# Performance work log

Hardware: AMD Instinct MI355X
Metric: run time of the kernel (lower is better)

Reference implementation:

```python
import jax, jax.numpy as jnp
import numpy as np


def setup_inputs() -> dict:
    key = jax.random.key(0)
    kq, kk, kv, kl = jax.random.split(key, 4)
    B, H, S, D = 2, 8, 1024, 64
    Q = jax.random.normal(kq, (B, H, S, D), dtype=jnp.float32)
    K = jax.random.normal(kk, (B, H, S, D), dtype=jnp.float32)
    V = jax.random.normal(kv, (B, H, S, D), dtype=jnp.float32)
    valid_lens = jax.random.randint(kl, (B, S), 0, S, dtype=jnp.int64)
    return {"Q": Q, "K": K, "V": V, "valid_lens": valid_lens}


def reference(Q, K, V, valid_lens):
    # Q,K,V: [B,H,S,D]. The torch repeat/reshape makes K[b,i,j]=K[b,j],
    # i.e. every query head i attends to every key/value head j.
    B, H, S, D = Q.shape
    inv_sqrt = 1.0 / jnp.sqrt(jnp.asarray(D, dtype=Q.dtype))
    # score[b,i,j,s,t] = Q[b,i,s,:] . K[b,j,t,:] / sqrt(D)
    score = jnp.einsum('bisd,bjtd->bijst', Q, K) * inv_sqrt
    attention_weights = jax.nn.softmax(score, axis=-1)  # [B,H,H,S,S]
    # ctx[b,i,s,d] = sum_j sum_t w[b,i,j,s,t] * V[b,j,t,d]  (matmul then sum over j)
    ctx = jnp.einsum('bijst,bjtd->bisd', attention_weights, V)  # [B,H,S,D]
    context = jnp.transpose(ctx, (0, 2, 1, 3)).reshape(B, S, H * D)  # [B,S,H*D]
    return context, attention_weights
```

## Files before the change

### kernel.cpp

```cpp
#include <hip/hip_runtime.h>
#include <hip/hip_bf16.h>

#define B_ 2
#define H_ 8
#define S_ 1024
#define D_ 64
#define PLP 136
#define STRIPH (16 * PLP)

typedef short short8 __attribute__((ext_vector_type(8)));
typedef float f32x4 __attribute__((ext_vector_type(4)));
typedef float f32x2 __attribute__((ext_vector_type(2)));

__device__ __forceinline__ unsigned int f2bf(float f) {
  union { float f; unsigned int u; } v; v.f = f;
  return (v.u + 0x7fffu + ((v.u >> 16) & 1u)) >> 16;
}
__device__ __forceinline__ float bf2f(unsigned int bits) {
  union { unsigned int u; float f; } v; v.u = bits << 16;
  return v.f;
}
__device__ __forceinline__ unsigned int cvt_pk_bf16(float lo, float hi) {
  unsigned int r;
  asm("v_cvt_pk_bf16_f32 %0, %1, %2" : "=v"(r) : "v"(lo), "v"(hi));
  return r;
}

__global__ void conv_bf16_kernel(const float* __restrict__ src,
                                 unsigned short* __restrict__ dst, int n4) {
  int idx = blockIdx.x * blockDim.x + threadIdx.x;
  if (idx >= n4) return;
  const float4 v = ((const float4*)src)[idx];
  unsigned int lo = f2bf(v.x) | (f2bf(v.y) << 16);
  unsigned int hi = f2bf(v.z) | (f2bf(v.w) << 16);
  ((uint2*)dst)[idx] = make_uint2(lo, hi);
}

__global__ void transpose_v_kernel(const float* __restrict__ V,
                                   unsigned short* __restrict__ Vt) {
  __shared__ float tile[64][65];
  int bh = blockIdx.x >> 4;
  int t0 = (blockIdx.x & 15) * 64;
  int tid = threadIdx.x;
  int cx = tid & 63, ry = tid >> 6;
  const float* src = V + ((size_t)bh * S_ + t0) * D_;
#pragma unroll
  for (int r = 0; r < 16; ++r) {
    int row = r * 4 + ry;
    tile[row][cx] = src[(size_t)row * D_ + cx];
  }
  __syncthreads();
  unsigned short* dst = Vt + (size_t)bh * D_ * S_ + t0;
#pragma unroll
  for (int r = 0; r < 16; ++r) {
    int d = r * 4 + ry;
    dst[(size_t)d * S_ + cx] = (unsigned short)f2bf(tile[cx][d]);
  }
}

__global__ __launch_bounds__(512, 2) void attn_kernel(
    const unsigned short* __restrict__ Qb,
    const unsigned short* __restrict__ Kb,
    const unsigned short* __restrict__ Vt,
    float* __restrict__ w_out,
    float* __restrict__ ctx_out)
{
  const int tid  = threadIdx.x;
  const int w    = tid >> 6;
  const int lane = tid & 63;
  const int g = lane >> 4;
  const int c = lane & 15;
  const int raw = blockIdx.x;
  const int bid = (raw & 7) * 32 + (raw >> 3);
  const int sb = bid & 15;
  const int i  = (bid >> 4) & 7;
  const int b  = bid >> 7;
  const int s0 = sb * 64;
  const int t0 = w * 128;

  __shared__ __align__(16) unsigned short pstrips[32 * STRIPH];
  __shared__ float ssum[2][8][64];
  unsigned short* stripA = pstrips + (4 * w) * STRIPH;
  unsigned short* stripB = stripA + STRIPH;
  unsigned short* stripC = stripB + STRIPH;
  unsigned short* stripD = stripC + STRIPH;

  const unsigned short* qrow =
      Qb + ((size_t)((b * H_ + i) * S_) + s0 + c) * D_ + g * 8;
  short8 qa0 = *(const short8*)(qrow);
  short8 qa1 = *(const short8*)(qrow + 32);
  short8 qb0 = *(const short8*)(qrow + 16 * D_);
  short8 qb1 = *(const short8*)(qrow + 16 * D_ + 32);
  short8 qc0 = *(const short8*)(qrow + 32 * D_);
  short8 qc1 = *(const short8*)(qrow + 32 * D_ + 32);
  short8 qd0 = *(const short8*)(qrow + 48 * D_);
  short8 qd1 = *(const short8*)(qrow + 48 * D_ + 32);

  f32x4 ctxA[4], ctxB[4], ctxC[4], ctxD[4];
#pragma unroll
  for (int nt = 0; nt < 4; ++nt) {
    ctxA[nt] = (f32x4){0.f, 0.f, 0.f, 0.f};
    ctxB[nt] = (f32x4){0.f, 0.f, 0.f, 0.f};
    ctxC[nt] = (f32x4){0.f, 0.f, 0.f, 0.f};
    ctxD[nt] = (f32x4){0.f, 0.f, 0.f, 0.f};
  }

  const float SC = 0.18033688011112042f;

  for (int j = 0; j < H_; ++j) {
    const int par = j & 1;
    const unsigned short* kbase = Kb + (size_t)((b * H_ + j) * S_) * D_;

    float rsA = 0.f, rsB = 0.f, rsC = 0.f, rsD = 0.f;
#pragma unroll
    for (int tt = 0; tt < 8; ++tt) {
      const unsigned short* kr = kbase + (size_t)(t0 + tt * 16 + c) * D_ + g * 8;
      short8 kf0 = *(const short8*)(kr);
      short8 kf1 = *(const short8*)(kr + 32);
#define PASS1_HALF(QF0, QF1, RS, STRIPP)                                      \
      {                                                                       \
        f32x4 acc = (f32x4){0.f, 0.f, 0.f, 0.f};                              \
        acc = __builtin_amdgcn_mfma_f32_16x16x32_bf16(kf0, QF0, acc, 0, 0, 0);\
        acc = __builtin_amdgcn_mfma_f32_16x16x32_bf16(kf1, QF1, acc, 0, 0, 0);\
        float e0 = exp2f(acc[0] * SC);                                        \
        float e1 = exp2f(acc[1] * SC);                                        \
        float e2 = exp2f(acc[2] * SC);                                        \
        float e3 = exp2f(acc[3] * SC);                                        \
        RS += (e0 + e1) + (e2 + e3);                                          \
        uint2 pk = make_uint2(cvt_pk_bf16(e0, e1), cvt_pk_bf16(e2, e3));      \
        *(uint2*)&STRIPP[c * PLP + tt * 16 + 4 * g] = pk;                     \
      }
      PASS1_HALF(qa0, qa1, rsA, stripA)
      PASS1_HALF(qb0, qb1, rsB, stripB)
      PASS1_HALF(qc0, qc1, rsC, stripC)
      PASS1_HALF(qd0, qd1, rsD, stripD)
#undef PASS1_HALF
    }
    rsA += __shfl_xor(rsA, 16, 64);
    rsA += __shfl_xor(rsA, 32, 64);
    rsB += __shfl_xor(rsB, 16, 64);
    rsB += __shfl_xor(rsB, 32, 64);
    rsC += __shfl_xor(rsC, 16, 64);
    rsC += __shfl_xor(rsC, 32, 64);
    rsD += __shfl_xor(rsD, 16, 64);
    rsD += __shfl_xor(rsD, 32, 64);
    if (lane < 16) {
      ssum[par][w][lane]      = rsA;
      ssum[par][w][16 + lane] = rsB;
      ssum[par][w][32 + lane] = rsC;
      ssum[par][w][48 + lane] = rsD;
    }

    f32x4 pvA[4], pvB[4], pvC[4], pvD[4];
#pragma unroll
    for (int nt = 0; nt < 4; ++nt) {
      pvA[nt] = (f32x4){0.f, 0.f, 0.f, 0.f};
      pvB[nt] = (f32x4){0.f, 0.f, 0.f, 0.f};
      pvC[nt] = (f32x4){0.f, 0.f, 0.f, 0.f};
      pvD[nt] = (f32x4){0.f, 0.f, 0.f, 0.f};
    }
    const unsigned short* vbase =
        Vt + ((size_t)((b * H_ + j) * D_) + c) * S_ + t0 + g * 8;
#pragma unroll
    for (int ch = 0; ch < 4; ++ch) {
      short8 paA = *(const short8*)&stripA[c * PLP + ch * 32 + g * 8];
      short8 paB = *(const short8*)&stripB[c * PLP + ch * 32 + g * 8];
      short8 paC = *(const short8*)&stripC[c * PLP + ch * 32 + g * 8];
      short8 paD = *(const short8*)&stripD[c * PLP + ch * 32 + g * 8];
#pragma unroll
      for (int nt = 0; nt < 4; ++nt) {
        short8 vf = *(const short8*)(vbase + (size_t)nt * 16 * S_ + ch * 32);
        pvA[nt] = __builtin_amdgcn_mfma_f32_16x16x32_bf16(paA, vf, pvA[nt], 0, 0, 0);
        pvB[nt] = __builtin_amdgcn_mfma_f32_16x16x32_bf16(paB, vf, pvB[nt], 0, 0, 0);
        pvC[nt] = __builtin_amdgcn_mfma_f32_16x16x32_bf16(paC, vf, pvC[nt], 0, 0, 0);
        pvD[nt] = __builtin_amdgcn_mfma_f32_16x16x32_bf16(paD, vf, pvD[nt], 0, 0, 0);
      }
    }

    asm volatile("s_waitcnt lgkmcnt(0)\n\ts_barrier" ::: "memory");

#define ROWSUM(OFS)                                                           \
    (ssum[par][0][(OFS) + c] + ssum[par][1][(OFS) + c] +                      \
     ssum[par][2][(OFS) + c] + ssum[par][3][(OFS) + c] +                      \
     ssum[par][4][(OFS) + c] + ssum[par][5][(OFS) + c] +                      \
     ssum[par][6][(OFS) + c] + ssum[par][7][(OFS) + c])
    float iqA = 1.f / ROWSUM(0);
    float iqB = 1.f / ROWSUM(16);
    float iqC = 1.f / ROWSUM(32);
    float iqD = 1.f / ROWSUM(48);
#undef ROWSUM

#define CTX_SCALE(IQ, PV, CTX)                                                \
    {                                                                         \
      float r0 = __shfl(IQ, 4 * g + 0, 64);                                   \
      float r1 = __shfl(IQ, 4 * g + 1, 64);                                   \
      float r2 = __shfl(IQ, 4 * g + 2, 64);                                   \
      float r3 = __shfl(IQ, 4 * g + 3, 64);                                   \
      _Pragma("unroll")                                                       \
      for (int nt = 0; nt < 4; ++nt) {                                        \
        CTX[nt][0] += PV[nt][0] * r0;                                         \
        CTX[nt][1] += PV[nt][1] * r1;                                         \
        CTX[nt][2] += PV[nt][2] * r2;                                         \
        CTX[nt][3] += PV[nt][3] * r3;                                         \
      }                                                                       \
    }
    CTX_SCALE(iqA, pvA, ctxA)
    CTX_SCALE(iqB, pvB, ctxB)
    CTX_SCALE(iqC, pvC, ctxC)
    CTX_SCALE(iqD, pvD, ctxD)
#undef CTX_SCALE

    float* wbase = w_out +
        ((size_t)((b * H_ + i) * H_ + j) * S_ + s0) * S_ + t0 + lane * 2;
#define WSTORE_HALF(IQ, STRIPP, ROWOFS)                                       \
    _Pragma("unroll")                                                         \
    for (int rr = 0; rr < 16; ++rr) {                                         \
      const float iq =                                                        \
          __uint_as_float(__builtin_amdgcn_readlane(__float_as_uint(IQ), rr));\
      unsigned int pk = *(const unsigned int*)&STRIPP[rr * PLP + lane * 2];   \
      f32x2 ww;                                                               \
      ww[0] = bf2f(pk & 0xffffu) * iq;                                        \
      ww[1] = bf2f(pk >> 16)     * iq;                                        \
      __builtin_nontemporal_store(                                            \
          ww, (f32x2*)(wbase + (size_t)((ROWOFS) + rr) * S_));                \
    }
    WSTORE_HALF(iqA, stripA, 0)
    WSTORE_HALF(iqB, stripB, 16)
    WSTORE_HALF(iqC, stripC, 32)
    WSTORE_HALF(iqD, stripD, 48)
#undef WSTORE_HALF
  }

  __syncthreads();
  float (*ctile)[64][68] = (float(*)[64][68])pstrips;
#pragma unroll
  for (int nt = 0; nt < 4; ++nt)
#pragma unroll
    for (int r = 0; r < 4; ++r) {
      ctile[w][4 * g + r][nt * 16 + c]      = ctxA[nt][r];
      ctile[w][16 + 4 * g + r][nt * 16 + c] = ctxB[nt][r];
      ctile[w][32 + 4 * g + r][nt * 16 + c] = ctxC[nt][r];
      ctile[w][48 + 4 * g + r][nt * 16 + c] = ctxD[nt][r];
    }
  __syncthreads();
#pragma unroll
  for (int it = 0; it < 2; ++it) {
    const int slot = it * 512 + tid;
    const int r  = slot >> 4;
    const int d0 = (slot & 15) * 4;
    f32x4 s = *(const f32x4*)&ctile[0][r][d0];
#pragma unroll
    for (int e = 1; e < 8; ++e) s += *(const f32x4*)&ctile[e][r][d0];
    *(f32x4*)(ctx_out + ((size_t)(b * S_ + s0 + r) * (H_ * D_) + i * D_ + d0)) = s;
  }
}

extern "C" void kernel_launch(void* const* d_in, const int* in_sizes, int n_in,
                              void* d_out, int out_size, void* d_ws, size_t ws_size,
                              hipStream_t stream) {
  const float* Q = (const float*)d_in[0];
  const float* K = (const float*)d_in[1];
  const float* V = (const float*)d_in[2];

  const size_t nelem = (size_t)B_ * H_ * S_ * D_;
  float* outc = (float*)d_out;
  float* outw = outc + (size_t)B_ * S_ * H_ * D_;

  unsigned short* Qb = (unsigned short*)d_ws;
  unsigned short* Kb = Qb + nelem;
  unsigned short* Vt = Kb + nelem;

  conv_bf16_kernel<<<1024, 256, 0, stream>>>(Q, Qb, (int)(nelem / 4));
  conv_bf16_kernel<<<1024, 256, 0, stream>>>(K, Kb, (int)(nelem / 4));
  transpose_v_kernel<<<256, 256, 0, stream>>>(V, Vt);

  attn_kernel<<<B_ * H_ * (S_ / 64), 512, 0, stream>>>(Qb, Kb, Vt, outw, outc);
}
```

Baseline: 157.6 us.

## Fuse prologue kernels and interleave weight stores with PV MFMAs

Merges the two bf16 conversion kernels and the V transpose into a single prologue launch, removing two kernel launches. In the attention kernel, the row-sum barrier and reciprocal now come before the PV matmul, and the normalized attention-weight stores are issued per chunk between the MFMA groups. The aim is to overlap the large global write stream with tensor-core work. Stores also widen from 2-float to 4-float nontemporal writes covering two rows per wave. The price is a longer barrier wait before the PV work and extra readlane/select logic per store.

```diff
diff --git a/kernel.cpp b/kernel.cpp
--- a/kernel.cpp
+++ b/kernel.cpp
@@ -10,7 +10,6 @@
 
 typedef short short8 __attribute__((ext_vector_type(8)));
 typedef float f32x4 __attribute__((ext_vector_type(4)));
-typedef float f32x2 __attribute__((ext_vector_type(2)));
 
 __device__ __forceinline__ unsigned int f2bf(float f) {
   union { float f; unsigned int u; } v; v.f = f;
@@ -26,21 +25,27 @@
   return r;
 }
 
-__global__ void conv_bf16_kernel(const float* __restrict__ src,
-                                 unsigned short* __restrict__ dst, int n4) {
-  int idx = blockIdx.x * blockDim.x + threadIdx.x;
-  if (idx >= n4) return;
-  const float4 v = ((const float4*)src)[idx];
-  unsigned int lo = f2bf(v.x) | (f2bf(v.y) << 16);
-  unsigned int hi = f2bf(v.z) | (f2bf(v.w) << 16);
-  ((uint2*)dst)[idx] = make_uint2(lo, hi);
-}
-
-__global__ void transpose_v_kernel(const float* __restrict__ V,
-                                   unsigned short* __restrict__ Vt) {
+__global__ void prologue_kernel(const float* __restrict__ Q,
+                                const float* __restrict__ K,
+                                const float* __restrict__ V,
+                                unsigned short* __restrict__ Qb,
+                                unsigned short* __restrict__ Kb,
+                                unsigned short* __restrict__ Vt) {
   __shared__ float tile[64][65];
-  int bh = blockIdx.x >> 4;
-  int t0 = (blockIdx.x & 15) * 64;
+  const int bid = blockIdx.x;
+  if (bid < 2048) {
+    const float* src = (bid < 1024) ? Q : K;
+    unsigned short* dst = (bid < 1024) ? Qb : Kb;
+    int idx = (bid & 1023) * 256 + threadIdx.x;
+    const float4 v = ((const float4*)src)[idx];
+    unsigned int lo = f2bf(v.x) | (f2bf(v.y) << 16);
+    unsigned int hi = f2bf(v.z) | (f2bf(v.w) << 16);
+    ((uint2*)dst)[idx] = make_uint2(lo, hi);
+    return;
+  }
+  const int tb = bid - 2048;
+  int bh = tb >> 4;
+  int t0 = (tb & 15) * 64;
   int tid = threadIdx.x;
   int cx = tid & 63, ry = tid >> 6;
   const float* src = V + ((size_t)bh * S_ + t0) * D_;
@@ -84,6 +89,10 @@
   unsigned short* stripB = stripA + STRIPH;
   unsigned short* stripC = stripB + STRIPH;
   unsigned short* stripD = stripC + STRIPH;
+
+  const int l5  = lane >> 5;
+  const int l31 = lane & 31;
+  const int soff = l5 * PLP + l31 * 4;
 
   const unsigned short* qrow =
       Qb + ((size_t)((b * H_ + i) * S_) + s0 + c) * D_ + g * 8;
@@ -151,32 +160,6 @@
       ssum[par][w][48 + lane] = rsD;
     }
 
-    f32x4 pvA[4], pvB[4], pvC[4], pvD[4];
-#pragma unroll
-    for (int nt = 0; nt < 4; ++nt) {
-      pvA[nt] = (f32x4){0.f, 0.f, 0.f, 0.f};
-      pvB[nt] = (f32x4){0.f, 0.f, 0.f, 0.f};
-      pvC[nt] = (f32x4){0.f, 0.f, 0.f, 0.f};
-      pvD[nt] = (f32x4){0.f, 0.f, 0.f, 0.f};
-    }
-    const unsigned short* vbase =
-        Vt + ((size_t)((b * H_ + j) * D_) + c) * S_ + t0 + g * 8;
-#pragma unroll
-    for (int ch = 0; ch < 4; ++ch) {
-      short8 paA = *(const short8*)&stripA[c * PLP + ch * 32 + g * 8];
-      short8 paB = *(const short8*)&stripB[c * PLP + ch * 32 + g * 8];
-      short8 paC = *(const short8*)&stripC[c * PLP + ch * 32 + g * 8];
-      short8 paD = *(const short8*)&stripD[c * PLP + ch * 32 + g * 8];
-#pragma unroll
-      for (int nt = 0; nt < 4; ++nt) {
-        short8 vf = *(const short8*)(vbase + (size_t)nt * 16 * S_ + ch * 32);
-        pvA[nt] = __builtin_amdgcn_mfma_f32_16x16x32_bf16(paA, vf, pvA[nt], 0, 0, 0);
-        pvB[nt] = __builtin_amdgcn_mfma_f32_16x16x32_bf16(paB, vf, pvB[nt], 0, 0, 0);
-        pvC[nt] = __builtin_amdgcn_mfma_f32_16x16x32_bf16(paC, vf, pvC[nt], 0, 0, 0);
-        pvD[nt] = __builtin_amdgcn_mfma_f32_16x16x32_bf16(paD, vf, pvD[nt], 0, 0, 0);
-      }
-    }
-
     asm volatile("s_waitcnt lgkmcnt(0)\n\ts_barrier" ::: "memory");
 
 #define ROWSUM(OFS)                                                           \
@@ -189,6 +172,54 @@
     float iqC = 1.f / ROWSUM(32);
     float iqD = 1.f / ROWSUM(48);
 #undef ROWSUM
+
+    f32x4 pvA[4], pvB[4], pvC[4], pvD[4];
+#pragma unroll
+    for (int nt = 0; nt < 4; ++nt) {
+      pvA[nt] = (f32x4){0.f, 0.f, 0.f, 0.f};
+      pvB[nt] = (f32x4){0.f, 0.f, 0.f, 0.f};
+      pvC[nt] = (f32x4){0.f, 0.f, 0.f, 0.f};
+      pvD[nt] = (f32x4){0.f, 0.f, 0.f, 0.f};
+    }
+    const unsigned short* vbase =
+        Vt + ((size_t)((b * H_ + j) * D_) + c) * S_ + t0 + g * 8;
+    float* wlane = w_out +
+        ((size_t)((b * H_ + i) * H_ + j) * S_ + s0) * S_ + t0 +
+        (size_t)l5 * S_ + l31 * 4;
+#pragma unroll
+    for (int ch = 0; ch < 4; ++ch) {
+      short8 paA = *(const short8*)&stripA[c * PLP + ch * 32 + g * 8];
+      short8 paB = *(const short8*)&stripB[c * PLP + ch * 32 + g * 8];
+      short8 paC = *(const short8*)&stripC[c * PLP + ch * 32 + g * 8];
+      short8 paD = *(const short8*)&stripD[c * PLP + ch * 32 + g * 8];
+#pragma unroll
+      for (int nt = 0; nt < 4; ++nt) {
+        short8 vf = *(const short8*)(vbase + (size_t)nt * 16 * S_ + ch * 32);
+        pvA[nt] = __builtin_amdgcn_mfma_f32_16x16x32_bf16(paA, vf, pvA[nt], 0, 0, 0);
+        pvB[nt] = __builtin_amdgcn_mfma_f32_16x16x32_bf16(paB, vf, pvB[nt], 0, 0, 0);
+        pvC[nt] = __builtin_amdgcn_mfma_f32_16x16x32_bf16(paC, vf, pvC[nt], 0, 0, 0);
+        pvD[nt] = __builtin_amdgcn_mfma_f32_16x16x32_bf16(paD, vf, pvD[nt], 0, 0, 0);
+      }
+      const float iqh = (ch == 0) ? iqA : (ch == 1) ? iqB : (ch == 2) ? iqC : iqD;
+      const unsigned short* sh =
+          (ch == 0) ? stripA : (ch == 1) ? stripB : (ch == 2) ? stripC : stripD;
+      float* wch = wlane + (size_t)(ch * 16) * S_;
+#pragma unroll
+      for (int q = 0; q < 8; ++q) {
+        float s0v = __uint_as_float(
+            __builtin_amdgcn_readlane(__float_as_uint(iqh), 2 * q));
+        float s1v = __uint_as_float(
+            __builtin_amdgcn_readlane(__float_as_uint(iqh), 2 * q + 1));
+        float iql = (lane & 32) ? s1v : s0v;
+        uint2 pk = *(const uint2*)&sh[2 * q * PLP + soff];
+        f32x4 ww;
+        ww[0] = bf2f(pk.x & 0xffffu) * iql;
+        ww[1] = bf2f(pk.x >> 16)     * iql;
+        ww[2] = bf2f(pk.y & 0xffffu) * iql;
+        ww[3] = bf2f(pk.y >> 16)     * iql;
+        __builtin_nontemporal_store(ww, (f32x4*)(wch + (size_t)(2 * q) * S_));
+      }
+    }
 
 #define CTX_SCALE(IQ, PV, CTX)                                                \
     {                                                                         \
@@ -209,26 +240,6 @@
     CTX_SCALE(iqC, pvC, ctxC)
     CTX_SCALE(iqD, pvD, ctxD)
 #undef CTX_SCALE
-
-    float* wbase = w_out +
-        ((size_t)((b * H_ + i) * H_ + j) * S_ + s0) * S_ + t0 + lane * 2;
-#define WSTORE_HALF(IQ, STRIPP, ROWOFS)                                       \
-    _Pragma("unroll")                                                         \
-    for (int rr = 0; rr < 16; ++rr) {                                         \
-      const float iq =                                                        \
-          __uint_as_float(__builtin_amdgcn_readlane(__float_as_uint(IQ), rr));\
-      unsigned int pk = *(const unsigned int*)&STRIPP[rr * PLP + lane * 2];   \
-      f32x2 ww;                                                               \
-      ww[0] = bf2f(pk & 0xffffu) * iq;                                        \
-      ww[1] = bf2f(pk >> 16)     * iq;                                        \
-      __builtin_nontemporal_store(                                            \
-          ww, (f32x2*)(wbase + (size_t)((ROWOFS) + rr) * S_));                \
-    }
-    WSTORE_HALF(iqA, stripA, 0)
-    WSTORE_HALF(iqB, stripB, 16)
-    WSTORE_HALF(iqC, stripC, 32)
-    WSTORE_HALF(iqD, stripD, 48)
-#undef WSTORE_HALF
   }
 
   __syncthreads();
@@ -270,9 +281,6 @@
   unsigned short* Kb = Qb + nelem;
   unsigned short* Vt = Kb + nelem;
 
-  conv_bf16_kernel<<<1024, 256, 0, stream>>>(Q, Qb, (int)(nelem / 4));
-  conv_bf16_kernel<<<1024, 256, 0, stream>>>(K, Kb, (int)(nelem / 4));
-  transpose_v_kernel<<<256, 256, 0, stream>>>(V, Vt);
-
+  prologue_kernel<<<2304, 256, 0, stream>>>(Q, K, V, Qb, Kb, Vt);
   attn_kernel<<<B_ * H_ * (S_ / 64), 512, 0, stream>>>(Qb, Kb, Vt, outw, outc);
 }
```

After: 141.2 us (median of 2 runs). 10.4% less time.
